# Kernel optimization log

Measured on AMD Instinct MI355X. Metric: run time of the kernel, lower is better.

The kernel has to match this reference:

```python
import jax, jax.numpy as jnp
import numpy as np

B, T, D, H = 4, 2048, 1024, 16
HD = D // H  # head_dim = 64

def setup_inputs() -> dict:
    key = jax.random.key(0)
    k1, k2, k3 = jax.random.split(key, 3)
    s = 1.0 / np.sqrt(D)
    return {
        "x": jax.random.normal(k1, (B, T, D), dtype=jnp.float32),
        "w_qkv": jax.random.normal(k2, (D, 3 * D), dtype=jnp.float32) * s,
        "b_qkv": jnp.zeros((3 * D,), dtype=jnp.float32),
        "w_proj": jax.random.normal(k3, (D, D), dtype=jnp.float32) * s,
        "b_proj": jnp.zeros((D,), dtype=jnp.float32),
    }

def reference(x, w_qkv, b_qkv, w_proj, b_proj):
    b, t, c = x.shape
    qkv = x @ w_qkv + b_qkv                       # [B,T,3D]
    qkv = qkv.reshape(b, t, 3, H, HD)
    q, k, v = (jnp.transpose(qkv[:, :, i], (0, 2, 1, 3)) for i in range(3))  # [B,H,T,HD]
    scale = 1.0 / np.sqrt(HD)
    attn = jnp.einsum('bhqd,bhkd->bhqk', q, k) * scale  # [B,H,T,T]
    attn = jax.nn.softmax(attn, axis=-1)
    out = jnp.einsum('bhqk,bhkd->bhqd', attn, v)        # [B,H,T,HD]
    out = jnp.transpose(out, (0, 2, 1, 3)).reshape(b, t, c)
    return out @ w_proj + b_proj
```

## Files before the change

### kernel.cpp

```cpp
#include <hip/hip_runtime.h>
#include <hip/hip_bf16.h>

#define T_SEQ   2048
#define D_MODEL 1024
#define N_HEADS 16
#define HEAD_DIM 64
#define BT      8192
#define N3D     3072

using short8  = __attribute__((ext_vector_type(8))) short;
using short4v = __attribute__((ext_vector_type(4))) short;
using floatx4 = __attribute__((ext_vector_type(4))) float;

#define QSCALE 0.18033688f

__device__ __forceinline__ unsigned short rne_bf16(float f) {
  unsigned int u = __float_as_uint(f);
  u = (u + 0x7fffu + ((u >> 16) & 1u)) >> 16;
  return (unsigned short)u;
}

__device__ __forceinline__ void gload_lds16(const unsigned short* g,
                                            unsigned short* l) {
  __builtin_amdgcn_global_load_lds(
      (const __attribute__((address_space(1))) void*)g,
      (__attribute__((address_space(3))) void*)l, 16, 0, 0);
}

__global__ __launch_bounds__(256) void k_convert(const float* __restrict__ in,
                                                 unsigned short* __restrict__ out) {
  size_t i = ((size_t)blockIdx.x * 256 + threadIdx.x) * 8;
  float4 a = *(const float4*)(in + i);
  float4 b = *(const float4*)(in + i + 4);
  short8 v;
  v[0] = (short)rne_bf16(a.x); v[1] = (short)rne_bf16(a.y);
  v[2] = (short)rne_bf16(a.z); v[3] = (short)rne_bf16(a.w);
  v[4] = (short)rne_bf16(b.x); v[5] = (short)rne_bf16(b.y);
  v[6] = (short)rne_bf16(b.z); v[7] = (short)rne_bf16(b.w);
  *(short8*)(((short*)out) + i) = v;
}

__global__ __launch_bounds__(256) void k_transpose_convert(
    const float* __restrict__ in, unsigned short* __restrict__ out_hi,
    int R, int C) {
  __shared__ float tile[64][65];
  int tiles_c = C >> 6;
  int r0 = (blockIdx.x / tiles_c) << 6;
  int c0 = (blockIdx.x % tiles_c) << 6;
  int tid = threadIdx.x;
#pragma unroll
  for (int i = 0; i < 16; ++i) {
    int idx = tid + i * 256;
    int r = idx >> 6, c = idx & 63;
    tile[r][c] = in[(size_t)(r0 + r) * C + c0 + c];
  }
  __syncthreads();
#pragma unroll
  for (int i = 0; i < 16; ++i) {
    int idx = tid + i * 256;
    int orow = idx >> 6, oc = idx & 63;
    out_hi[(size_t)(c0 + orow) * R + r0 + oc] = rne_bf16(tile[oc][orow]);
  }
}

__global__ __launch_bounds__(256) void k_qkv_gemm(
    const unsigned short* __restrict__ A, const unsigned short* __restrict__ Bt,
    const float* __restrict__ bias,
    unsigned short* __restrict__ Qo, unsigned short* __restrict__ Ko,
    unsigned short* __restrict__ Vt) {
  __shared__ __align__(16) unsigned short As[128 * 32];
  __shared__ __align__(16) unsigned short Bs[128 * 32];
  int tid = threadIdx.x;
  int m0 = (blockIdx.x / 24) * 128;
  int n0 = (blockIdx.x % 24) * 128;
  int w = tid >> 6, lane = tid & 63, quad = lane >> 4, l16 = lane & 15;
  int wm = (w >> 1) * 64, wn = (w & 1) * 64;
  floatx4 acc[4][4] = {};

  int s_row[2], s_sp[2];
#pragma unroll
  for (int i = 0; i < 2; ++i) {
    int u = tid + i * 256;
    s_row[i] = u >> 2;
    s_sp[i] = (u & 3) ^ ((s_row[i] >> 1) & 3);
  }
  int a_off[4], b_off[4];
#pragma unroll
  for (int t = 0; t < 4; ++t) {
    int ra = wm + t * 16 + l16, rb = wn + t * 16 + l16;
    a_off[t] = ra * 32 + (quad ^ ((ra >> 1) & 3)) * 8;
    b_off[t] = rb * 32 + (quad ^ ((rb >> 1) & 3)) * 8;
  }

  for (int k0 = 0; k0 < 1024; k0 += 32) {
#pragma unroll
    for (int i = 0; i < 2; ++i) {
      int ub = (tid & ~63) + i * 256;
      gload_lds16(A + (size_t)(m0 + s_row[i]) * 1024 + k0 + s_sp[i] * 8,
                  &As[ub * 8]);
      gload_lds16(Bt + (size_t)(n0 + s_row[i]) * 1024 + k0 + s_sp[i] * 8,
                  &Bs[ub * 8]);
    }
    __syncthreads();
    short8 af[4], bf[4];
#pragma unroll
    for (int mt = 0; mt < 4; ++mt) af[mt] = *(const short8*)(&As[a_off[mt]]);
#pragma unroll
    for (int nt = 0; nt < 4; ++nt) bf[nt] = *(const short8*)(&Bs[b_off[nt]]);
#pragma unroll
    for (int mt = 0; mt < 4; ++mt)
#pragma unroll
      for (int nt = 0; nt < 4; ++nt)
        acc[mt][nt] = __builtin_amdgcn_mfma_f32_16x16x32_bf16(af[mt], bf[nt],
                                                              acc[mt][nt], 0, 0, 0);
    __syncthreads();
  }

#pragma unroll
  for (int nt = 0; nt < 4; ++nt) {
    int n = n0 + wn + nt * 16 + l16;
    float bv = bias[n];
    int which = n >> 10;
    int nn = n & 1023;
    int h = nn >> 6, hd = nn & 63;
#pragma unroll
    for (int mt = 0; mt < 4; ++mt) {
      int mbase = m0 + wm + mt * 16 + quad * 4;
      int b = mbase >> 11;
      int t0 = mbase & 2047;
      int head = b * N_HEADS + h;
      if (which == 2) {
        short4v vv;
#pragma unroll
        for (int r = 0; r < 4; ++r) vv[r] = (short)rne_bf16(acc[mt][nt][r] + bv);
        *(short4v*)(&Vt[((size_t)head * HEAD_DIM + hd) * T_SEQ + t0]) = vv;
      } else {
        unsigned short* dst = (which == 0) ? Qo : Ko;
        float scl = (which == 0) ? QSCALE : 1.0f;
#pragma unroll
        for (int r = 0; r < 4; ++r)
          dst[((size_t)head * T_SEQ + t0 + r) * HEAD_DIM + hd] =
              rne_bf16((acc[mt][nt][r] + bv) * scl);
      }
    }
  }
}

__global__ __launch_bounds__(256) void k_attn(
    const unsigned short* __restrict__ Q, const unsigned short* __restrict__ K,
    const unsigned short* __restrict__ Vt, unsigned short* __restrict__ Oo) {
  __shared__ __align__(16) unsigned short Klds[64 * 64];
  __shared__ __align__(16) unsigned short Vlds[64 * 64];
  int tid = threadIdx.x;
  int head = blockIdx.x >> 4;
  int qb = (blockIdx.x & 15) << 7;
  int b = head >> 4, h = head & 15;
  int w = tid >> 6, lane = tid & 63, quad = lane >> 4, l16 = lane & 15;
  const unsigned short* Qh = Q + (size_t)head * T_SEQ * HEAD_DIM;
  const unsigned short* Kh = K + (size_t)head * T_SEQ * HEAD_DIM;
  const unsigned short* Vh = Vt + (size_t)head * HEAD_DIM * T_SEQ;

  short8 qf[2][2];
#pragma unroll
  for (int qi = 0; qi < 2; ++qi) {
    int qrow = qb + w * 32 + qi * 16 + l16;
#pragma unroll
    for (int ks = 0; ks < 2; ++ks)
      qf[qi][ks] = *(const short8*)(Qh + (size_t)qrow * 64 + ks * 32 + quad * 8);
  }

  short8 ones;
#pragma unroll
  for (int j = 0; j < 8; ++j) ones[j] = (short)0x3F80;

  floatx4 O[2][4] = {};
  floatx4 Osum[2] = {};
  const floatx4 zf = {};

  int sg[2], sub[2], ksrc[2], vsrc[2];
#pragma unroll
  for (int i = 0; i < 2; ++i) {
    sg[i] = (tid + i * 256) >> 6;
    sub[i] = (tid & ~63) + i * 256;
    int xs = lane ^ sg[i];
    int ntp = xs >> 4, mp = xs & 15;
    ksrc[i] = ((ntp >> 1) << 5) + ((mp >> 2) << 3) + ((ntp & 1) << 2) + (mp & 3);
    vsrc[i] = xs;
  }

  for (int kb = 0; kb < 32; ++kb) {
#pragma unroll
    for (int i = 0; i < 2; ++i) {
      gload_lds16(Kh + ((size_t)(kb * 64 + ksrc[i])) * 64 + sg[i] * 8,
                  &Klds[sub[i] * 8]);
      gload_lds16(Vh + (size_t)vsrc[i] * T_SEQ + kb * 64 + sg[i] * 8,
                  &Vlds[sub[i] * 8]);
    }
    __syncthreads();

    floatx4 s[2][4];
#pragma unroll
    for (int ks = 0; ks < 2; ++ks) {
      int gk = ks * 4 + quad;
#pragma unroll
      for (int nt = 0; nt < 4; ++nt) {
        int PU = ((gk << 6) + nt * 16 + l16) ^ gk;
        short8 kf = *(const short8*)(&Klds[PU * 8]);
        if (ks == 0) {
          s[0][nt] = __builtin_amdgcn_mfma_f32_16x16x32_bf16(kf, qf[0][0], zf, 0, 0, 0);
          s[1][nt] = __builtin_amdgcn_mfma_f32_16x16x32_bf16(kf, qf[1][0], zf, 0, 0, 0);
        } else {
          s[0][nt] = __builtin_amdgcn_mfma_f32_16x16x32_bf16(kf, qf[0][1], s[0][nt], 0, 0, 0);
          s[1][nt] = __builtin_amdgcn_mfma_f32_16x16x32_bf16(kf, qf[1][1], s[1][nt], 0, 0, 0);
        }
      }
    }

    short8 pB[2][2];
#pragma unroll
    for (int qi = 0; qi < 2; ++qi) {
      unsigned int dw[4][2];
#pragma unroll
      for (int nt = 0; nt < 4; ++nt) {
        float p0 = __builtin_amdgcn_exp2f(s[qi][nt][0]);
        float p1 = __builtin_amdgcn_exp2f(s[qi][nt][1]);
        float p2 = __builtin_amdgcn_exp2f(s[qi][nt][2]);
        float p3 = __builtin_amdgcn_exp2f(s[qi][nt][3]);
        __hip_bfloat162 lo2 = __float22bfloat162_rn(make_float2(p0, p1));
        __hip_bfloat162 hi2 = __float22bfloat162_rn(make_float2(p2, p3));
        dw[nt][0] = *(unsigned int*)&lo2;
        dw[nt][1] = *(unsigned int*)&hi2;
      }
#pragma unroll
      for (int ks = 0; ks < 2; ++ks) {
        union { unsigned int u[4]; short8 s8; } cv;
        cv.u[0] = dw[2 * ks][0];
        cv.u[1] = dw[2 * ks][1];
        cv.u[2] = dw[2 * ks + 1][0];
        cv.u[3] = dw[2 * ks + 1][1];
        pB[qi][ks] = cv.s8;
      }
    }

#pragma unroll
    for (int ks = 0; ks < 2; ++ks) {
      int gk = ks * 4 + quad;
      Osum[0] = __builtin_amdgcn_mfma_f32_16x16x32_bf16(ones, pB[0][ks], Osum[0], 0, 0, 0);
      Osum[1] = __builtin_amdgcn_mfma_f32_16x16x32_bf16(ones, pB[1][ks], Osum[1], 0, 0, 0);
#pragma unroll
      for (int dt = 0; dt < 4; ++dt) {
        int PUv = ((gk << 6) + dt * 16 + l16) ^ gk;
        short8 vf = *(const short8*)(&Vlds[PUv * 8]);
        O[0][dt] = __builtin_amdgcn_mfma_f32_16x16x32_bf16(vf, pB[0][ks], O[0][dt], 0, 0, 0);
        O[1][dt] = __builtin_amdgcn_mfma_f32_16x16x32_bf16(vf, pB[1][ks], O[1][dt], 0, 0, 0);
      }
    }
    __syncthreads();
  }

#pragma unroll
  for (int qi = 0; qi < 2; ++qi) {
    float inv = 1.0f / Osum[qi][0];
    int t = qb + w * 32 + qi * 16 + l16;
    size_t rowo = ((size_t)(b * T_SEQ + t)) * D_MODEL + h * HEAD_DIM;
#pragma unroll
    for (int dt = 0; dt < 4; ++dt) {
      short4v ov;
#pragma unroll
      for (int r = 0; r < 4; ++r) ov[r] = (short)rne_bf16(O[qi][dt][r] * inv);
      *(short4v*)(&Oo[rowo + dt * 16 + quad * 4]) = ov;
    }
  }
}

__global__ __launch_bounds__(256) void k_proj_gemm(
    const unsigned short* __restrict__ A, const unsigned short* __restrict__ Bt,
    const float* __restrict__ bias, float* __restrict__ out) {
  __shared__ __align__(16) unsigned short As[128 * 32];
  __shared__ __align__(16) unsigned short Bs[128 * 32];
  int tid = threadIdx.x;
  int m0 = (blockIdx.x >> 3) * 128;
  int n0 = (blockIdx.x & 7) * 128;
  int w = tid >> 6, lane = tid & 63, quad = lane >> 4, l16 = lane & 15;
  int wm = (w >> 1) * 64, wn = (w & 1) * 64;
  floatx4 acc[4][4] = {};

  int s_row[2], s_sp[2];
#pragma unroll
  for (int i = 0; i < 2; ++i) {
    int u = tid + i * 256;
    s_row[i] = u >> 2;
    s_sp[i] = (u & 3) ^ ((s_row[i] >> 1) & 3);
  }
  int a_off[4], b_off[4];
#pragma unroll
  for (int t = 0; t < 4; ++t) {
    int ra = wm + t * 16 + l16, rb = wn + t * 16 + l16;
    a_off[t] = ra * 32 + (quad ^ ((ra >> 1) & 3)) * 8;
    b_off[t] = rb * 32 + (quad ^ ((rb >> 1) & 3)) * 8;
  }

  for (int k0 = 0; k0 < 1024; k0 += 32) {
#pragma unroll
    for (int i = 0; i < 2; ++i) {
      int ub = (tid & ~63) + i * 256;
      gload_lds16(A + (size_t)(m0 + s_row[i]) * 1024 + k0 + s_sp[i] * 8,
                  &As[ub * 8]);
      gload_lds16(Bt + (size_t)(n0 + s_row[i]) * 1024 + k0 + s_sp[i] * 8,
                  &Bs[ub * 8]);
    }
    __syncthreads();
    short8 af[4], bf[4];
#pragma unroll
    for (int mt = 0; mt < 4; ++mt) af[mt] = *(const short8*)(&As[a_off[mt]]);
#pragma unroll
    for (int nt = 0; nt < 4; ++nt) bf[nt] = *(const short8*)(&Bs[b_off[nt]]);
#pragma unroll
    for (int mt = 0; mt < 4; ++mt)
#pragma unroll
      for (int nt = 0; nt < 4; ++nt)
        acc[mt][nt] = __builtin_amdgcn_mfma_f32_16x16x32_bf16(af[mt], bf[nt],
                                                              acc[mt][nt], 0, 0, 0);
    __syncthreads();
  }

#pragma unroll
  for (int nt = 0; nt < 4; ++nt) {
    int n = n0 + wn + nt * 16 + l16;
    float bv = bias[n];
#pragma unroll
    for (int mt = 0; mt < 4; ++mt)
#pragma unroll
      for (int r = 0; r < 4; ++r) {
        int m = m0 + wm + mt * 16 + quad * 4 + r;
        out[(size_t)m * 1024 + n] = acc[mt][nt][r] + bv;
      }
  }
}

extern "C" void kernel_launch(void* const* d_in, const int* in_sizes, int n_in,
                              void* d_out, int out_size, void* d_ws, size_t ws_size,
                              hipStream_t stream) {
  const float* x     = (const float*)d_in[0];
  const float* wqkv  = (const float*)d_in[1];
  const float* bqkv  = (const float*)d_in[2];
  const float* wproj = (const float*)d_in[3];
  const float* bproj = (const float*)d_in[4];

  char* ws = (char*)d_ws;
  size_t off = 0;
  unsigned short* x_bf  = (unsigned short*)(ws + off); off += (size_t)BT * D_MODEL * 2;
  unsigned short* wq_T  = (unsigned short*)(ws + off); off += (size_t)N3D * D_MODEL * 2;
  unsigned short* wp_T  = (unsigned short*)(ws + off); off += (size_t)D_MODEL * D_MODEL * 2;
  unsigned short* Qb    = (unsigned short*)(ws + off); off += (size_t)BT * D_MODEL * 2;
  unsigned short* Kb    = (unsigned short*)(ws + off); off += (size_t)BT * D_MODEL * 2;
  unsigned short* Vt    = (unsigned short*)(ws + off); off += (size_t)BT * D_MODEL * 2;
  unsigned short* a_bf  = (unsigned short*)(ws + off); off += (size_t)BT * D_MODEL * 2;

  k_convert<<<(BT * D_MODEL) / (256 * 8), 256, 0, stream>>>(x, x_bf);
  k_transpose_convert<<<(1024 / 64) * (3072 / 64), 256, 0, stream>>>(wqkv, wq_T, 1024, 3072);
  k_transpose_convert<<<(1024 / 64) * (1024 / 64), 256, 0, stream>>>(wproj, wp_T, 1024, 1024);
  k_qkv_gemm<<<(BT / 128) * (N3D / 128), 256, 0, stream>>>(x_bf, wq_T, bqkv, Qb, Kb, Vt);
  k_attn<<<(T_SEQ / 128) * 4 * N_HEADS, 256, 0, stream>>>(Qb, Kb, Vt, a_bf);
  k_proj_gemm<<<(BT / 128) * (D_MODEL / 128), 256, 0, stream>>>(a_bf, wp_T, bproj, (float*)d_out);
}
```

Baseline: 329.4 us.

## Double-buffer K/V tiles in attention kernel to overlap loads with MFMA compute

The attention kernel now uses two LDS buffers for K and V. The next tile's global-to-LDS load is issued before computing on the current tile, which replaces the load-then-sync-then-compute pattern and halves the barriers per tile. LDS swizzle offsets are precomputed once outside the loop, and s_setprio raises wave priority around the MFMA sections. LDS use doubles (32KB per block), which could reduce occupancy.

```diff
diff --git a/kernel.cpp b/kernel.cpp
--- a/kernel.cpp
+++ b/kernel.cpp
@@ -149,8 +149,8 @@
 __global__ __launch_bounds__(256) void k_attn(
     const unsigned short* __restrict__ Q, const unsigned short* __restrict__ K,
     const unsigned short* __restrict__ Vt, unsigned short* __restrict__ Oo) {
-  __shared__ __align__(16) unsigned short Klds[64 * 64];
-  __shared__ __align__(16) unsigned short Vlds[64 * 64];
+  __shared__ __align__(16) unsigned short Klds[2][64 * 64];
+  __shared__ __align__(16) unsigned short Vlds[2][64 * 64];
   int tid = threadIdx.x;
   int head = blockIdx.x >> 4;
   int qb = (blockIdx.x & 15) << 7;
@@ -188,24 +188,33 @@
     vsrc[i] = xs;
   }
 
-  for (int kb = 0; kb < 32; ++kb) {
+  int pu[2][4];
+#pragma unroll
+  for (int ks = 0; ks < 2; ++ks) {
+    int gk = ks * 4 + quad;
+#pragma unroll
+    for (int t = 0; t < 4; ++t)
+      pu[ks][t] = (((gk << 6) + t * 16 + l16) ^ gk) << 3;
+  }
+
+  auto stage = [&](int buf, int kb) {
 #pragma unroll
     for (int i = 0; i < 2; ++i) {
       gload_lds16(Kh + ((size_t)(kb * 64 + ksrc[i])) * 64 + sg[i] * 8,
-                  &Klds[sub[i] * 8]);
+                  &Klds[buf][sub[i] * 8]);
       gload_lds16(Vh + (size_t)vsrc[i] * T_SEQ + kb * 64 + sg[i] * 8,
-                  &Vlds[sub[i] * 8]);
-    }
-    __syncthreads();
-
+                  &Vlds[buf][sub[i] * 8]);
+    }
+  };
+
+  auto compute = [&](const unsigned short* Kb_, const unsigned short* Vb_) {
     floatx4 s[2][4];
+    __builtin_amdgcn_s_setprio(1);
 #pragma unroll
     for (int ks = 0; ks < 2; ++ks) {
-      int gk = ks * 4 + quad;
 #pragma unroll
       for (int nt = 0; nt < 4; ++nt) {
-        int PU = ((gk << 6) + nt * 16 + l16) ^ gk;
-        short8 kf = *(const short8*)(&Klds[PU * 8]);
+        short8 kf = *(const short8*)(Kb_ + pu[ks][nt]);
         if (ks == 0) {
           s[0][nt] = __builtin_amdgcn_mfma_f32_16x16x32_bf16(kf, qf[0][0], zf, 0, 0, 0);
           s[1][nt] = __builtin_amdgcn_mfma_f32_16x16x32_bf16(kf, qf[1][0], zf, 0, 0, 0);
@@ -215,6 +224,7 @@
         }
       }
     }
+    __builtin_amdgcn_s_setprio(0);
 
     short8 pB[2][2];
 #pragma unroll
@@ -244,17 +254,29 @@
 
 #pragma unroll
     for (int ks = 0; ks < 2; ++ks) {
-      int gk = ks * 4 + quad;
+      __builtin_amdgcn_s_setprio(1);
       Osum[0] = __builtin_amdgcn_mfma_f32_16x16x32_bf16(ones, pB[0][ks], Osum[0], 0, 0, 0);
       Osum[1] = __builtin_amdgcn_mfma_f32_16x16x32_bf16(ones, pB[1][ks], Osum[1], 0, 0, 0);
 #pragma unroll
       for (int dt = 0; dt < 4; ++dt) {
-        int PUv = ((gk << 6) + dt * 16 + l16) ^ gk;
-        short8 vf = *(const short8*)(&Vlds[PUv * 8]);
+        short8 vf = *(const short8*)(Vb_ + pu[ks][dt]);
         O[0][dt] = __builtin_amdgcn_mfma_f32_16x16x32_bf16(vf, pB[0][ks], O[0][dt], 0, 0, 0);
         O[1][dt] = __builtin_amdgcn_mfma_f32_16x16x32_bf16(vf, pB[1][ks], O[1][dt], 0, 0, 0);
       }
-    }
+      __builtin_amdgcn_s_setprio(0);
+    }
+  };
+
+  stage(0, 0);
+  __syncthreads();
+
+#pragma unroll 1
+  for (int kb = 0; kb < 32; kb += 2) {
+    stage(1, kb + 1);
+    compute(&Klds[0][0], &Vlds[0][0]);
+    __syncthreads();
+    if (kb + 2 < 32) stage(0, kb + 2);
+    compute(&Klds[1][0], &Vlds[1][0]);
     __syncthreads();
   }
 
```

Result: faster. 310.8 us (-5.6%).
